# Optimization experiments

Measured on AMD Instinct MI355X. Metric: run time of the kernel, lower is better.

The kernel has to match this reference:

```python
import jax, jax.numpy as jnp
import numpy as np

N, E, D_IN, D_E, D_OUT = 100000, 1250000, 64, 64, 64


def setup_inputs() -> dict:
    key = jax.random.key(0)
    ks = jax.random.split(key, 8)
    return {
        "nfeats": jax.random.normal(ks[0], (N, 1, D_IN), dtype=jnp.float32),
        "efeats": jax.random.normal(ks[1], (E, 1, D_E), dtype=jnp.float32),
        "src": jax.random.randint(ks[2], (E,), 0, N, dtype=jnp.int32),
        "dst": jax.random.randint(ks[3], (E,), 0, N, dtype=jnp.int32),
        "W_msg": jax.random.normal(ks[4], (D_OUT, D_IN + D_E), dtype=jnp.float32) * 0.08,
        "b_msg": jax.random.normal(ks[5], (D_OUT,), dtype=jnp.float32) * 0.02,
        "W_apply": jax.random.normal(ks[6], (D_OUT, D_IN + D_OUT), dtype=jnp.float32) * 0.08,
        "b_apply": jax.random.normal(ks[7], (D_OUT,), dtype=jnp.float32) * 0.02,
    }


def reference(nfeats, efeats, src, dst, W_msg, b_msg, W_apply, b_apply):
    n = nfeats.shape[0]
    # per-edge message: Linear(cat(src_h, edge_h))  -> [E, 1, D_OUT]
    edge_in = jnp.concatenate([nfeats[src], efeats], axis=-1)  # [E,1,D_IN+D_E]
    m = jnp.einsum('ekd,od->eko', edge_in, W_msg) + b_msg
    # mean segment-reduce over destination nodes (empty segments -> 0, like DGL mean)
    msum = jax.ops.segment_sum(m, dst, num_segments=n)  # [N,1,D_OUT]
    cnt = jax.ops.segment_sum(jnp.ones((dst.shape[0],), dtype=m.dtype), dst, num_segments=n)
    h_neigh = msum / jnp.maximum(cnt, 1.0)[:, None, None]
    # apply: relu(Linear(cat(h, h_neigh)))
    node_in = jnp.concatenate([nfeats, h_neigh], axis=-1)  # [N,1,D_IN+D_OUT]
    return jax.nn.relu(jnp.einsum('nkd,od->nko', node_in, W_apply) + b_apply)
```

## Files before the change

kernel.cpp:

```cpp
#include <hip/hip_runtime.h>
#include <hip/hip_bf16.h>


typedef __attribute__((ext_vector_type(8))) short bf16x8;
typedef __attribute__((ext_vector_type(4))) float f32x4;

__device__ __forceinline__ short f2bf(float f) {
  union { float f; unsigned u; } v; v.f = f;
  unsigned u = v.u;
  u += 0x7fffu + ((u >> 16) & 1u);
  return (short)(u >> 16);
}

__device__ __forceinline__ bf16x8 pack8(float4 a, float4 b) {
  bf16x8 r;
  r[0] = f2bf(a.x); r[1] = f2bf(a.y); r[2] = f2bf(a.z); r[3] = f2bf(a.w);
  r[4] = f2bf(b.x); r[5] = f2bf(b.y); r[6] = f2bf(b.z); r[7] = f2bf(b.w);
  return r;
}

__global__ __launch_bounds__(256) void prep_k(
    const float* __restrict__ nf, const float* __restrict__ Wm,
    const float* __restrict__ Wa, short* __restrict__ nf16,
    short* __restrict__ wpack, int conv_blocks, long total_nf)
{
  if ((int)blockIdx.x < conv_blocks) {
    long t = (long)blockIdx.x * 256 + threadIdx.x;
    long b8 = t * 8;
    if (b8 + 8 <= total_nf) {
      const float* p = nf + b8;
      *(bf16x8*)(nf16 + b8) = pack8(*(const float4*)p, *(const float4*)(p + 4));
    }
  } else {
    int t = threadIdx.x;
#pragma unroll
    for (int j = 0; j < 8; ++j) {
      int id = t * 8 + j;
      int w = id >> 10, kc = (id >> 8) & 3, nc = (id >> 6) & 3, lane = id & 63;
      int r = lane & 15, g = lane >> 4;
      const float* W = w ? Wa : Wm;
      const float* p = W + (nc * 16 + r) * 128 + kc * 32 + g * 8;
      *(bf16x8*)(wpack + (long)id * 8) = pack8(*(const float4*)p, *(const float4*)(p + 4));
    }
  }
}

__global__ __launch_bounds__(256) void hist_k(const int* __restrict__ dst,
                                              int* __restrict__ hist, int E) {
  int i = blockIdx.x * blockDim.x + threadIdx.x;
  int stride = gridDim.x * blockDim.x;
  for (; i < E; i += stride) atomicAdd(&hist[dst[i]], 1);
}

__global__ __launch_bounds__(256) void scan1_k(const int* __restrict__ hist,
                                               int* __restrict__ off,
                                               int* __restrict__ parts, int N) {
  __shared__ int sh[256];
  int tid = threadIdx.x;
  int base = blockIdx.x * 1024 + tid * 4;
  int v[4], ts = 0;
#pragma unroll
  for (int j = 0; j < 4; ++j) {
    int idx = base + j;
    v[j] = (idx < N) ? hist[idx] : 0;
    ts += v[j];
  }
  sh[tid] = ts;
  __syncthreads();
  for (int o = 1; o < 256; o <<= 1) {
    int y = (tid >= o) ? sh[tid - o] : 0;
    __syncthreads();
    sh[tid] += y;
    __syncthreads();
  }
  int run = sh[tid] - ts;
#pragma unroll
  for (int j = 0; j < 4; ++j) {
    int idx = base + j;
    if (idx < N) off[idx] = run;
    run += v[j];
  }
  if (tid == 255) parts[blockIdx.x] = sh[255];
}

__global__ void scan2_k(int* __restrict__ parts, int* __restrict__ off,
                        int nparts, int N, int E) {
  int lane = threadIdx.x & 63;
  int i0 = 2 * lane, i1 = 2 * lane + 1;
  int p0 = (i0 < nparts) ? parts[i0] : 0;
  int p1 = (i1 < nparts) ? parts[i1] : 0;
  int s = p0 + p1;
  int x = s;
  for (int o = 1; o < 64; o <<= 1) {
    int y = __shfl_up(x, o);
    if (lane >= o) x += y;
  }
  int ex = x - s;
  if (i0 < nparts) parts[i0] = ex;
  if (i1 < nparts) parts[i1] = ex + p0;
  if (lane == 0) off[N] = E;
}

__global__ __launch_bounds__(256) void scan3_k(int* __restrict__ off,
                                               int* __restrict__ woff,
                                               const int* __restrict__ parts, int N) {
  int p = parts[blockIdx.x];
  int base = blockIdx.x * 1024 + threadIdx.x;
#pragma unroll
  for (int j = 0; j < 4; ++j) {
    int idx = base + j * 256;
    if (idx < N) {
      int v = off[idx] + p;
      off[idx] = v;
      woff[idx] = v;
    }
  }
}

__global__ __launch_bounds__(256) void bin_k(
    const int* __restrict__ src, const int* __restrict__ dst,
    int* __restrict__ woff, int* __restrict__ seid, int* __restrict__ ssrc, int E) {
  int i = blockIdx.x * blockDim.x + threadIdx.x;
  int stride = gridDim.x * blockDim.x;
  for (; i < E; i += stride) {
    int d = dst[i];
    int pos = atomicAdd(&woff[d], 1);
    seid[pos] = i;
    ssrc[pos] = src[i];
  }
}

__global__ __launch_bounds__(256) void reduce_k(
    const float* __restrict__ nf, const float* __restrict__ ef,
    const int* __restrict__ off, const int* __restrict__ seid,
    const int* __restrict__ ssrc, short* __restrict__ ssum16, int N)
{
  int wave = (blockIdx.x * blockDim.x + threadIdx.x) >> 6;
  int lane = threadIdx.x & 63;
  if (wave >= N) return;
  int beg = off[wave], end = off[wave + 1];
  float anf = 0.f, aef = 0.f;
  int i = beg;
  for (; i + 1 < end; i += 2) {
    int s0 = ssrc[i], s1 = ssrc[i + 1];
    int e0 = seid[i], e1 = seid[i + 1];
    float x0 = nf[(size_t)s0 * 64 + lane];
    float x1 = nf[(size_t)s1 * 64 + lane];
    float y0 = ef[(size_t)e0 * 64 + lane];
    float y1 = ef[(size_t)e1 * 64 + lane];
    anf += x0 + x1;
    aef += y0 + y1;
  }
  if (i < end) {
    anf += nf[(size_t)ssrc[i] * 64 + lane];
    aef += ef[(size_t)seid[i] * 64 + lane];
  }
  short* row = ssum16 + (size_t)wave * 128;
  row[lane] = f2bf(anf);
  row[64 + lane] = f2bf(aef);
}

__global__ __launch_bounds__(256) void node_apply(
    const short* __restrict__ nf16, const short* __restrict__ ssum16,
    const int* __restrict__ off, const short* __restrict__ wpack,
    const float* __restrict__ b_msg, const float* __restrict__ b_apply,
    float* __restrict__ out, int ntiles)
{
  __shared__ float hn[4][16 * 68];
  const int wid = threadIdx.x >> 6;
  const int lane = threadIdx.x & 63;
  const int r = lane & 15;
  const int g = lane >> 4;
  const int tile = blockIdx.x * 4 + wid;
  if (tile >= ntiles) return;
  const int n0 = tile * 16;

  bf16x8 wm[4][4], wa[4][4];
#pragma unroll
  for (int kc = 0; kc < 4; ++kc)
#pragma unroll
    for (int nc = 0; nc < 4; ++nc) {
      wm[kc][nc] = *(const bf16x8*)(wpack + ((long)((0 * 4 + kc) * 4 + nc) * 64 + lane) * 8);
      wa[kc][nc] = *(const bf16x8*)(wpack + ((long)((1 * 4 + kc) * 4 + nc) * 64 + lane) * 8);
    }

  f32x4 acc[4] = {};
#pragma unroll
  for (int kc = 0; kc < 4; ++kc) {
    const bf16x8 af = *(const bf16x8*)(ssum16 + (size_t)(n0 + r) * 128 + kc * 32 + g * 8);
#pragma unroll
    for (int nc = 0; nc < 4; ++nc)
      acc[nc] = __builtin_amdgcn_mfma_f32_16x16x32_bf16(af, wm[kc][nc], acc[nc], 0, 0, 0);
  }

  float cn[4];
#pragma unroll
  for (int q = 0; q < 4; ++q) {
    int n = n0 + g * 4 + q;
    cn[q] = (float)(off[n + 1] - off[n]);
  }
#pragma unroll
  for (int nc = 0; nc < 4; ++nc) {
    const float bm = b_msg[nc * 16 + r];
#pragma unroll
    for (int q = 0; q < 4; ++q) {
      const float v = cn[q] > 0.f ? acc[nc][q] / cn[q] + bm : 0.f;
      hn[wid][(g * 4 + q) * 68 + nc * 16 + r] = v;
    }
  }

  f32x4 acc2[4] = {};
#pragma unroll
  for (int kc = 0; kc < 2; ++kc) {
    const bf16x8 af = *(const bf16x8*)(nf16 + (size_t)(n0 + r) * 64 + kc * 32 + g * 8);
#pragma unroll
    for (int nc = 0; nc < 4; ++nc)
      acc2[nc] = __builtin_amdgcn_mfma_f32_16x16x32_bf16(af, wa[kc][nc], acc2[nc], 0, 0, 0);
  }
#pragma unroll
  for (int kc = 2; kc < 4; ++kc) {
    const float* p = &hn[wid][r * 68 + (kc - 2) * 32 + g * 8];
    const bf16x8 af = pack8(*(const float4*)p, *(const float4*)(p + 4));
#pragma unroll
    for (int nc = 0; nc < 4; ++nc)
      acc2[nc] = __builtin_amdgcn_mfma_f32_16x16x32_bf16(af, wa[kc][nc], acc2[nc], 0, 0, 0);
  }

#pragma unroll
  for (int nc = 0; nc < 4; ++nc) {
    const float ba = b_apply[nc * 16 + r];
#pragma unroll
    for (int q = 0; q < 4; ++q) {
      float v = acc2[nc][q] + ba;
      v = v > 0.f ? v : 0.f;
      out[(size_t)(n0 + g * 4 + q) * 64 + nc * 16 + r] = v;
    }
  }
}

extern "C" void kernel_launch(void* const* d_in, const int* in_sizes, int n_in,
                              void* d_out, int out_size, void* d_ws, size_t ws_size,
                              hipStream_t stream) {
  const float* nfeats  = (const float*)d_in[0];
  const float* efeats  = (const float*)d_in[1];
  const int*   src     = (const int*)d_in[2];
  const int*   dst     = (const int*)d_in[3];
  const float* W_msg   = (const float*)d_in[4];
  const float* b_msg   = (const float*)d_in[5];
  const float* W_apply = (const float*)d_in[6];
  const float* b_apply = (const float*)d_in[7];
  float* out = (float*)d_out;

  const int N = in_sizes[0] / 64;
  const int E = in_sizes[2];
  const int nparts = (N + 1023) / 1024;

  auto alignup = [](size_t x) { return (x + 127) & ~(size_t)127; };
  char* ws = (char*)d_ws;
  size_t o = 0;
  int* hist   = (int*)(ws + o); o = alignup(o + (size_t)N * 4);
  int* off    = (int*)(ws + o); o = alignup(o + (size_t)(N + 1) * 4);
  int* woff   = (int*)(ws + o); o = alignup(o + (size_t)N * 4);
  int* parts  = (int*)(ws + o); o = alignup(o + (size_t)nparts * 4);
  int* seid   = (int*)(ws + o); o = alignup(o + (size_t)E * 4);
  int* ssrc   = (int*)(ws + o); o = alignup(o + (size_t)E * 4);
  short* ssum16 = (short*)(ws + o); o = alignup(o + (size_t)N * 128 * 2);
  short* nf16   = (short*)(ws + o); o = alignup(o + (size_t)N * 64 * 2);
  short* wpack  = (short*)(ws + o); o = alignup(o + (size_t)2048 * 8 * 2);

  hipMemsetAsync(hist, 0, (size_t)N * 4, stream);

  const long total_nf = (long)N * 64;
  const int conv_blocks = (int)((total_nf / 8 + 255) / 256);
  prep_k<<<conv_blocks + 1, 256, 0, stream>>>(nfeats, W_msg, W_apply, nf16, wpack,
                                              conv_blocks, total_nf);
  hist_k<<<1024, 256, 0, stream>>>(dst, hist, E);
  scan1_k<<<nparts, 256, 0, stream>>>(hist, off, parts, N);
  scan2_k<<<1, 64, 0, stream>>>(parts, off, nparts, N, E);
  scan3_k<<<nparts, 256, 0, stream>>>(off, woff, parts, N);
  bin_k<<<1024, 256, 0, stream>>>(src, dst, woff, seid, ssrc, E);
  reduce_k<<<(N + 3) / 4, 256, 0, stream>>>(nfeats, efeats, off, seid, ssrc, ssum16, N);

  const int ntiles = (N + 15) / 16;
  node_apply<<<(ntiles + 3) / 4, 256, 0, stream>>>(nf16, ssum16, off, wpack,
                                                   b_msg, b_apply, out, ntiles);
}
```

Before: 694.9 us.

## Fuse histogram into prep kernel, pack edge ids, vectorize gather-reduce

Merges the dst histogram into the prep kernel so one launch does both. The separate edge-id and source-id arrays become one int2 array, so binning does one scattered write per edge and the reduce does one index load. The reduce now has each quarter-wave handle a different edge with float4 loads, processing four edges per iteration, and combines the partial sums with cross-lane shuffles. The cost is extra shuffle work and lanes sitting idle on the tail of low-degree nodes.

```diff
diff --git a/kernel.cpp b/kernel.cpp
--- a/kernel.cpp
+++ b/kernel.cpp
@@ -3,6 +3,7 @@
 
 
 typedef __attribute__((ext_vector_type(8))) short bf16x8;
+typedef __attribute__((ext_vector_type(4))) short bf16x4;
 typedef __attribute__((ext_vector_type(4))) float f32x4;
 
 __device__ __forceinline__ short f2bf(float f) {
@@ -19,19 +20,27 @@
   return r;
 }
 
-__global__ __launch_bounds__(256) void prep_k(
+__device__ __forceinline__ bf16x4 pack4(float4 a) {
+  bf16x4 r;
+  r[0] = f2bf(a.x); r[1] = f2bf(a.y); r[2] = f2bf(a.z); r[3] = f2bf(a.w);
+  return r;
+}
+
+__global__ __launch_bounds__(256) void prep_hist_k(
     const float* __restrict__ nf, const float* __restrict__ Wm,
     const float* __restrict__ Wa, short* __restrict__ nf16,
-    short* __restrict__ wpack, int conv_blocks, long total_nf)
+    short* __restrict__ wpack, const int* __restrict__ dst,
+    int* __restrict__ hist, int conv_blocks, long total_nf, int E, int hist_blocks)
 {
-  if ((int)blockIdx.x < conv_blocks) {
-    long t = (long)blockIdx.x * 256 + threadIdx.x;
+  const int bx = blockIdx.x;
+  if (bx < conv_blocks) {
+    long t = (long)bx * 256 + threadIdx.x;
     long b8 = t * 8;
     if (b8 + 8 <= total_nf) {
       const float* p = nf + b8;
       *(bf16x8*)(nf16 + b8) = pack8(*(const float4*)p, *(const float4*)(p + 4));
     }
-  } else {
+  } else if (bx == conv_blocks) {
     int t = threadIdx.x;
 #pragma unroll
     for (int j = 0; j < 8; ++j) {
@@ -42,14 +51,23 @@
       const float* p = W + (nc * 16 + r) * 128 + kc * 32 + g * 8;
       *(bf16x8*)(wpack + (long)id * 8) = pack8(*(const float4*)p, *(const float4*)(p + 4));
     }
-  }
-}
-
-__global__ __launch_bounds__(256) void hist_k(const int* __restrict__ dst,
-                                              int* __restrict__ hist, int E) {
-  int i = blockIdx.x * blockDim.x + threadIdx.x;
-  int stride = gridDim.x * blockDim.x;
-  for (; i < E; i += stride) atomicAdd(&hist[dst[i]], 1);
+  } else {
+    const int hb = bx - conv_blocks - 1;
+    int i4 = hb * 256 + threadIdx.x;
+    const int stride = hist_blocks * 256;
+    const int E4 = E >> 2;
+    for (; i4 < E4; i4 += stride) {
+      const int4 d = ((const int4*)dst)[i4];
+      atomicAdd(&hist[d.x], 1);
+      atomicAdd(&hist[d.y], 1);
+      atomicAdd(&hist[d.z], 1);
+      atomicAdd(&hist[d.w], 1);
+    }
+    if (hb == 0) {
+      int i = (E & ~3) + (int)threadIdx.x;
+      if (i < E) atomicAdd(&hist[dst[i]], 1);
+    }
+  }
 }
 
 __global__ __launch_bounds__(256) void scan1_k(const int* __restrict__ hist,
@@ -119,45 +137,76 @@
 
 __global__ __launch_bounds__(256) void bin_k(
     const int* __restrict__ src, const int* __restrict__ dst,
-    int* __restrict__ woff, int* __restrict__ seid, int* __restrict__ ssrc, int E) {
-  int i = blockIdx.x * blockDim.x + threadIdx.x;
-  int stride = gridDim.x * blockDim.x;
-  for (; i < E; i += stride) {
-    int d = dst[i];
-    int pos = atomicAdd(&woff[d], 1);
-    seid[pos] = i;
-    ssrc[pos] = src[i];
+    int* __restrict__ woff, int2* __restrict__ packed, int E) {
+  int i4 = blockIdx.x * blockDim.x + threadIdx.x;
+  const int stride = gridDim.x * blockDim.x;
+  const int E4 = E >> 2;
+  for (; i4 < E4; i4 += stride) {
+    const int4 d = ((const int4*)dst)[i4];
+    const int4 s = ((const int4*)src)[i4];
+    const int e0 = i4 * 4;
+    int p;
+    p = atomicAdd(&woff[d.x], 1); packed[p] = make_int2(e0 + 0, s.x);
+    p = atomicAdd(&woff[d.y], 1); packed[p] = make_int2(e0 + 1, s.y);
+    p = atomicAdd(&woff[d.z], 1); packed[p] = make_int2(e0 + 2, s.z);
+    p = atomicAdd(&woff[d.w], 1); packed[p] = make_int2(e0 + 3, s.w);
+  }
+  if (blockIdx.x == 0) {
+    int i = (E & ~3) + (int)threadIdx.x;
+    if (i < E) {
+      int p = atomicAdd(&woff[dst[i]], 1);
+      packed[p] = make_int2(i, src[i]);
+    }
   }
 }
 
 __global__ __launch_bounds__(256) void reduce_k(
     const float* __restrict__ nf, const float* __restrict__ ef,
-    const int* __restrict__ off, const int* __restrict__ seid,
-    const int* __restrict__ ssrc, short* __restrict__ ssum16, int N)
+    const int* __restrict__ off, const int2* __restrict__ packed,
+    short* __restrict__ ssum16, int N)
 {
-  int wave = (blockIdx.x * blockDim.x + threadIdx.x) >> 6;
-  int lane = threadIdx.x & 63;
+  const int wave = (blockIdx.x * blockDim.x + threadIdx.x) >> 6;
+  const int lane = threadIdx.x & 63;
   if (wave >= N) return;
-  int beg = off[wave], end = off[wave + 1];
-  float anf = 0.f, aef = 0.f;
+  const int g = lane >> 4;
+  const int s = lane & 15;
+  const int beg = off[wave], end = off[wave + 1];
+
+  float4 anf = make_float4(0.f, 0.f, 0.f, 0.f);
+  float4 aef = make_float4(0.f, 0.f, 0.f, 0.f);
+
   int i = beg;
-  for (; i + 1 < end; i += 2) {
-    int s0 = ssrc[i], s1 = ssrc[i + 1];
-    int e0 = seid[i], e1 = seid[i + 1];
-    float x0 = nf[(size_t)s0 * 64 + lane];
-    float x1 = nf[(size_t)s1 * 64 + lane];
-    float y0 = ef[(size_t)e0 * 64 + lane];
-    float y1 = ef[(size_t)e1 * 64 + lane];
-    anf += x0 + x1;
-    aef += y0 + y1;
-  }
-  if (i < end) {
-    anf += nf[(size_t)ssrc[i] * 64 + lane];
-    aef += ef[(size_t)seid[i] * 64 + lane];
-  }
+  const int nfull = (end - beg) & ~3;
+  for (; i < beg + nfull; i += 4) {
+    const int2 pk = packed[i + g];
+    const float4 x = *(const float4*)(nf + (size_t)pk.y * 64 + s * 4);
+    const float4 y = *(const float4*)(ef + (size_t)pk.x * 64 + s * 4);
+    anf.x += x.x; anf.y += x.y; anf.z += x.z; anf.w += x.w;
+    aef.x += y.x; aef.y += y.y; aef.z += y.z; aef.w += y.w;
+  }
+  const int rem = end - i;
+  if (g < rem) {
+    const int2 pk = packed[i + g];
+    const float4 x = *(const float4*)(nf + (size_t)pk.y * 64 + s * 4);
+    const float4 y = *(const float4*)(ef + (size_t)pk.x * 64 + s * 4);
+    anf.x += x.x; anf.y += x.y; anf.z += x.z; anf.w += x.w;
+    aef.x += y.x; aef.y += y.y; aef.z += y.z; aef.w += y.w;
+  }
+
+#pragma unroll
+  for (int m = 16; m <= 32; m <<= 1) {
+    anf.x += __shfl_xor(anf.x, m); anf.y += __shfl_xor(anf.y, m);
+    anf.z += __shfl_xor(anf.z, m); anf.w += __shfl_xor(anf.w, m);
+    aef.x += __shfl_xor(aef.x, m); aef.y += __shfl_xor(aef.y, m);
+    aef.z += __shfl_xor(aef.z, m); aef.w += __shfl_xor(aef.w, m);
+  }
+
   short* row = ssum16 + (size_t)wave * 128;
-  row[lane] = f2bf(anf);
-  row[64 + lane] = f2bf(aef);
+  if (g == 0) {
+    *(bf16x4*)(row + s * 4) = pack4(anf);
+  } else if (g == 1) {
+    *(bf16x4*)(row + 64 + s * 4) = pack4(aef);
+  }
 }
 
 __global__ __launch_bounds__(256) void node_apply(
@@ -245,8 +294,8 @@
   const float* efeats  = (const float*)d_in[1];
   const int*   src     = (const int*)d_in[2];
   const int*   dst     = (const int*)d_in[3];
+  const float* b_msg   = (const float*)d_in[5];
   const float* W_msg   = (const float*)d_in[4];
-  const float* b_msg   = (const float*)d_in[5];
   const float* W_apply = (const float*)d_in[6];
   const float* b_apply = (const float*)d_in[7];
   float* out = (float*)d_out;
@@ -258,12 +307,11 @@
   auto alignup = [](size_t x) { return (x + 127) & ~(size_t)127; };
   char* ws = (char*)d_ws;
   size_t o = 0;
-  int* hist   = (int*)(ws + o); o = alignup(o + (size_t)N * 4);
-  int* off    = (int*)(ws + o); o = alignup(o + (size_t)(N + 1) * 4);
-  int* woff   = (int*)(ws + o); o = alignup(o + (size_t)N * 4);
-  int* parts  = (int*)(ws + o); o = alignup(o + (size_t)nparts * 4);
-  int* seid   = (int*)(ws + o); o = alignup(o + (size_t)E * 4);
-  int* ssrc   = (int*)(ws + o); o = alignup(o + (size_t)E * 4);
+  int*  hist   = (int*)(ws + o);  o = alignup(o + (size_t)N * 4);
+  int*  off    = (int*)(ws + o);  o = alignup(o + (size_t)(N + 1) * 4);
+  int*  woff   = (int*)(ws + o);  o = alignup(o + (size_t)N * 4);
+  int*  parts  = (int*)(ws + o);  o = alignup(o + (size_t)nparts * 4);
+  int2* packed = (int2*)(ws + o); o = alignup(o + (size_t)E * 8);
   short* ssum16 = (short*)(ws + o); o = alignup(o + (size_t)N * 128 * 2);
   short* nf16   = (short*)(ws + o); o = alignup(o + (size_t)N * 64 * 2);
   short* wpack  = (short*)(ws + o); o = alignup(o + (size_t)2048 * 8 * 2);
@@ -272,14 +320,15 @@
 
   const long total_nf = (long)N * 64;
   const int conv_blocks = (int)((total_nf / 8 + 255) / 256);
-  prep_k<<<conv_blocks + 1, 256, 0, stream>>>(nfeats, W_msg, W_apply, nf16, wpack,
-                                              conv_blocks, total_nf);
-  hist_k<<<1024, 256, 0, stream>>>(dst, hist, E);
+  const int hist_blocks = 1024;
+  prep_hist_k<<<conv_blocks + 1 + hist_blocks, 256, 0, stream>>>(
+      nfeats, W_msg, W_apply, nf16, wpack, dst, hist,
+      conv_blocks, total_nf, E, hist_blocks);
   scan1_k<<<nparts, 256, 0, stream>>>(hist, off, parts, N);
   scan2_k<<<1, 64, 0, stream>>>(parts, off, nparts, N, E);
   scan3_k<<<nparts, 256, 0, stream>>>(off, woff, parts, N);
-  bin_k<<<1024, 256, 0, stream>>>(src, dst, woff, seid, ssrc, E);
-  reduce_k<<<(N + 3) / 4, 256, 0, stream>>>(nfeats, efeats, off, seid, ssrc, ssum16, N);
+  bin_k<<<1024, 256, 0, stream>>>(src, dst, woff, packed, E);
+  reduce_k<<<(N + 3) / 4, 256, 0, stream>>>(nfeats, efeats, off, packed, ssum16, N);
 
   const int ntiles = (N + 15) / 16;
   node_apply<<<(ntiles + 3) / 4, 256, 0, stream>>>(nf16, ssum16, off, wpack,
```

New measurement: 647.1 us. 6.9% less time.
